# Performance work log

Measured on AMD Instinct MI355X. Metric: run time of the kernel, lower is better.

The kernel has to match this reference:

```python
import jax, jax.numpy as jnp
import numpy as np

EPS = 1e-12  # torch F.normalize eps

def _l2norm(t):
    # F.normalize(t, p=2, dim=1): divide by clamped L2 norm
    n = jnp.sqrt(jnp.sum(t * t, axis=1, keepdims=True))
    return t / jnp.maximum(n, EPS)


def setup_inputs() -> dict:
    key = jax.random.key(0)
    k1, k2, k3 = jax.random.split(key, 3)
    N, K, D = 262144, 512, 64
    inputs = jax.random.normal(k1, (N, D), dtype=jnp.float32)
    labels = jax.random.randint(k2, (N,), 0, K, dtype=jnp.int64)
    embedding = jax.random.normal(k3, (K, D), dtype=jnp.float32)
    return {"inputs": inputs, "labels": labels, "embedding": embedding}


def reference(inputs, labels, embedding):
    K, D = embedding.shape
    flat = inputs.reshape(-1, D)  # [N, D]
    # cosine similarity: [N, K]
    distances = _l2norm(flat) @ _l2norm(embedding).T
    encoding_indices = jnp.argmax(distances, axis=1)  # [N]
    encodings = jax.nn.one_hot(encoding_indices, K, dtype=flat.dtype)  # [N, K]
    # quantize lookup via one-hot matmul (as in original)
    quantized = (encodings @ embedding).reshape(inputs.shape)
    # labeled branch: closs = mean(1 - distances[i, labels[i]])
    picked = jnp.take_along_axis(distances, labels[:, None], axis=1)[:, 0]
    loss = jnp.mean(1.0 - picked)
    # straight-through estimator
    quantized = inputs + jax.lax.stop_gradient(quantized - inputs)
    perplexity = jnp.array(1, dtype=jnp.int32)
    return (loss, quantized, perplexity, encodings, encoding_indices[:, None])
```

## Files before the change

kernel.cpp:

```cpp
#include <hip/hip_runtime.h>
#include <math.h>

#define N_ROWS 262144
#define KCODES 512
#define DIM 64
#define BLOCK 256
#define ROWS_PER_BLOCK 128
#define NSUB (KCODES / 16)


typedef __attribute__((ext_vector_type(8))) short short8;
typedef __attribute__((ext_vector_type(4))) float f4;

static const size_t OFF_LOSS = 0;
static const size_t OFF_Q    = 1;
static const size_t OFF_PERP = 1 + (size_t)N_ROWS * DIM;
static const size_t OFF_ENC  = OFF_PERP + 1;
static const size_t OFF_IDX  = OFF_ENC + (size_t)N_ROWS * KCODES;

__device__ __forceinline__ unsigned short bf16rne(float f) {
    unsigned int u = __float_as_uint(f);
    u = (u + 0x7fffu + ((u >> 16) & 1u)) >> 16;
    return (unsigned short)u;
}
__device__ __forceinline__ float bf16tof(unsigned short h) {
    return __uint_as_float(((unsigned int)h) << 16);
}

__global__ __launch_bounds__(64) void vq_prep(const float* __restrict__ emb,
                                              unsigned short* __restrict__ pe,
                                              float* __restrict__ out_loss,
                                              float* __restrict__ out_perp) {
    int k = blockIdx.x;
    int d = threadIdx.x;
    float v = emb[k * DIM + d];
    float s = v * v;
    #pragma unroll
    for (int off = 32; off > 0; off >>= 1) s += __shfl_xor(s, off, 64);
    float vn = v / fmaxf(sqrtf(s), 1e-12f);
    unsigned short h = bf16rne(vn);
    float r = vn - bf16tof(h);
    unsigned short m = bf16rne(r);
    r = r - bf16tof(m);
    unsigned short l = bf16rne(r);
    int st = k >> 4, cc = k & 15;
    int ss = d >> 5, qq = (d >> 3) & 3, j = d & 7;
    int ln = qq * 16 + cc;
    pe[((size_t)(st * 6 + 0 + ss) * 64 + ln) * 8 + j] = h;
    pe[((size_t)(st * 6 + 2 + ss) * 64 + ln) * 8 + j] = m;
    pe[((size_t)(st * 6 + 4 + ss) * 64 + ln) * 8 + j] = l;
    if (k == 0 && d == 0) { *out_loss = 0.0f; *out_perp = 1.0f; }
}

#define MFMA(A, B, C) C = __builtin_amdgcn_mfma_f32_16x16x32_bf16(A, B, C, 0, 0, 0)

__global__ __launch_bounds__(BLOCK, 3) void vq_main(const float* __restrict__ x,
                                                    const int* __restrict__ labels,
                                                    const float* __restrict__ emb,
                                                    const unsigned short* __restrict__ pe,
                                                    float* __restrict__ out_loss,
                                                    float* __restrict__ out_q,
                                                    float* __restrict__ out_enc,
                                                    float* __restrict__ out_idx) {
    const int tid   = threadIdx.x;
    const int lane  = tid & 63;
    const int q     = lane >> 4;
    const int c     = lane & 15;
    const int wbase = blockIdx.x * ROWS_PER_BLOCK + (tid >> 6) * 32;

    float inv_nx[2];
    short8 Ah[2][2], Am[2][2], Al[2][2];
    #pragma unroll
    for (int t = 0; t < 2; ++t) {
        float xv[16];
        const float* xp = x + (size_t)(wbase + t * 16 + c) * DIM + q * 8;
        #pragma unroll
        for (int s = 0; s < 2; ++s) {
            float4 lo = *(const float4*)(xp + s * 32);
            float4 hi = *(const float4*)(xp + s * 32 + 4);
            xv[s * 8 + 0] = lo.x; xv[s * 8 + 1] = lo.y;
            xv[s * 8 + 2] = lo.z; xv[s * 8 + 3] = lo.w;
            xv[s * 8 + 4] = hi.x; xv[s * 8 + 5] = hi.y;
            xv[s * 8 + 6] = hi.z; xv[s * 8 + 7] = hi.w;
        }
        float s2 = 0.f;
        #pragma unroll
        for (int j = 0; j < 16; ++j) s2 = fmaf(xv[j], xv[j], s2);
        s2 += __shfl_xor(s2, 16, 64);
        s2 += __shfl_xor(s2, 32, 64);
        inv_nx[t] = 1.0f / fmaxf(sqrtf(s2), 1e-12f);
        #pragma unroll
        for (int s = 0; s < 2; ++s)
            #pragma unroll
            for (int j = 0; j < 8; ++j) {
                float v = xv[s * 8 + j];
                unsigned short h = bf16rne(v);
                float r = v - bf16tof(h);
                unsigned short m = bf16rne(r);
                r = r - bf16tof(m);
                unsigned short l = bf16rne(r);
                Ah[t][s][j] = (short)h;
                Am[t][s][j] = (short)m;
                Al[t][s][j] = (short)l;
            }
    }

    int   lbl[2][4];
    float best[2][4], pick[2][4];
    int   bidx[2][4];
    #pragma unroll
    for (int t = 0; t < 2; ++t)
        #pragma unroll
        for (int r = 0; r < 4; ++r) {
            lbl[t][r]  = labels[wbase + t * 16 + q * 4 + r];
            best[t][r] = -3.4e38f;
            bidx[t][r] = 0;
            pick[t][r] = 0.f;
        }

    #pragma unroll 2
    for (int st = 0; st < NSUB; ++st) {
        const unsigned short* bp = pe + ((size_t)st * 6 * 64 + lane) * 8;
        short8 Bh0 = *(const short8*)(bp);
        short8 Bh1 = *(const short8*)(bp + 512);
        short8 Bm0 = *(const short8*)(bp + 1024);
        short8 Bm1 = *(const short8*)(bp + 1536);
        short8 Bl0 = *(const short8*)(bp + 2048);
        short8 Bl1 = *(const short8*)(bp + 2560);

        {
            float* zb = out_enc + (size_t)(wbase + st) * KCODES;
            f4 z = {0.f, 0.f, 0.f, 0.f};
            __builtin_nontemporal_store(z, (f4*)(zb + lane * 4));
            __builtin_nontemporal_store(z, (f4*)(zb + 256 + lane * 4));
        }

        f4 acc0 = {0.f, 0.f, 0.f, 0.f};
        f4 acc1 = {0.f, 0.f, 0.f, 0.f};
        MFMA(Ah[0][0], Bh0, acc0);  MFMA(Ah[1][0], Bh0, acc1);
        MFMA(Ah[0][1], Bh1, acc0);  MFMA(Ah[1][1], Bh1, acc1);
        MFMA(Ah[0][0], Bm0, acc0);  MFMA(Ah[1][0], Bm0, acc1);
        MFMA(Ah[0][1], Bm1, acc0);  MFMA(Ah[1][1], Bm1, acc1);
        MFMA(Am[0][0], Bh0, acc0);  MFMA(Am[1][0], Bh0, acc1);
        MFMA(Am[0][1], Bh1, acc0);  MFMA(Am[1][1], Bh1, acc1);
        MFMA(Ah[0][0], Bl0, acc0);  MFMA(Ah[1][0], Bl0, acc1);
        MFMA(Ah[0][1], Bl1, acc0);  MFMA(Ah[1][1], Bl1, acc1);
        MFMA(Al[0][0], Bh0, acc0);  MFMA(Al[1][0], Bh0, acc1);
        MFMA(Al[0][1], Bh1, acc0);  MFMA(Al[1][1], Bh1, acc1);
        MFMA(Am[0][0], Bm0, acc0);  MFMA(Am[1][0], Bm0, acc1);
        MFMA(Am[0][1], Bm1, acc0);  MFMA(Am[1][1], Bm1, acc1);

        const int code = st * 16 + c;
        #pragma unroll
        for (int r = 0; r < 4; ++r) {
            float d0 = acc0[r];
            if (d0 > best[0][r]) { best[0][r] = d0; bidx[0][r] = code; }
            if (code == lbl[0][r]) pick[0][r] = d0;
            float d1 = acc1[r];
            if (d1 > best[1][r]) { best[1][r] = d1; bidx[1][r] = code; }
            if (code == lbl[1][r]) pick[1][r] = d1;
        }
    }

    asm volatile("s_waitcnt vmcnt(0)" ::: "memory");

    #pragma unroll
    for (int t = 0; t < 2; ++t)
        #pragma unroll
        for (int r = 0; r < 4; ++r) {
            float b = best[t][r]; int i = bidx[t][r]; float p = pick[t][r];
            #pragma unroll
            for (int m = 1; m < 16; m <<= 1) {
                float ob = __shfl_xor(b, m, 64);
                int   oi = __shfl_xor(i, m, 64);
                p += __shfl_xor(p, m, 64);
                if (ob > b || (ob == b && oi < i)) { b = ob; i = oi; }
            }
            bidx[t][r] = i; pick[t][r] = p;
        }

    if (c == 0) {
        #pragma unroll
        for (int t = 0; t < 2; ++t)
            #pragma unroll
            for (int r = 0; r < 4; ++r) {
                int row = wbase + t * 16 + q * 4 + r;
                out_enc[(size_t)row * KCODES + bidx[t][r]] = 1.0f;
                out_idx[row] = (float)bidx[t][r];
            }
    }

    #pragma unroll
    for (int t = 0; t < 2; ++t)
        #pragma unroll
        for (int r = 0; r < 4; ++r) {
            int row = wbase + t * 16 + q * 4 + r;
            f4 v = ((const f4*)(emb + (size_t)bidx[t][r] * DIM))[c];
            __builtin_nontemporal_store(v, ((f4*)(out_q + (size_t)row * DIM)) + c);
        }

    float lv = 0.f;
    #pragma unroll
    for (int t = 0; t < 2; ++t)
        #pragma unroll
        for (int r = 0; r < 4; ++r) {
            float invv = __shfl(inv_nx[t], q * 4 + r, 64);
            lv += (1.0f - pick[t][r] * invv);
        }
    lv *= 1.0f / ((float)N_ROWS * 16.0f);
    #pragma unroll
    for (int m = 1; m < 64; m <<= 1) lv += __shfl_xor(lv, m, 64);
    if (lane == 0) atomicAdd(out_loss, lv);
}

extern "C" void kernel_launch(void* const* d_in, const int* in_sizes, int n_in,
                              void* d_out, int out_size, void* d_ws, size_t ws_size,
                              hipStream_t stream) {
    const float* x      = (const float*)d_in[0];
    const int*   labels = (const int*)d_in[1];
    const float* emb    = (const float*)d_in[2];
    float* out = (float*)d_out;
    unsigned short* pe = (unsigned short*)d_ws;

    hipLaunchKernelGGL(vq_prep, dim3(KCODES), dim3(64), 0, stream,
                       emb, pe, out + OFF_LOSS, out + OFF_PERP);
    hipLaunchKernelGGL(vq_main, dim3(N_ROWS / ROWS_PER_BLOCK), dim3(BLOCK), 0, stream,
                       x, labels, emb, pe,
                       out + OFF_LOSS, out + OFF_Q, out + OFF_ENC, out + OFF_IDX);
}
```

Baseline: 718.2 us.

## Stage codebook tiles in LDS and write one-hot rows after argmax

Codebook fragments are now loaded cooperatively into shared memory in stages of four 16-code subtiles, with block barriers, instead of each wave reading them from global memory. The separate zero-fill stores plus scattered 1.0 store for the encodings matrix become one pass that writes each one-hot row directly once the argmax is known. Occupancy hint raised from 3 to 6 blocks per SM. The aim is to cut redundant global/L2 traffic and remove the overlapping zero-then-set writes, at the cost of synchronization stalls, and it no longer overlaps the large encoding writes with the MFMA loop.

```diff
diff --git a/kernel.cpp b/kernel.cpp
--- a/kernel.cpp
+++ b/kernel.cpp
@@ -6,7 +6,10 @@
 #define DIM 64
 #define BLOCK 256
 #define ROWS_PER_BLOCK 128
-#define NSUB (KCODES / 16)
+#define NSUB 32
+#define SUBS_PER_STAGE 4
+#define NSTAGES (NSUB / SUBS_PER_STAGE)
+#define STAGE_USHORTS (SUBS_PER_STAGE * 6 * 64 * 8)
 
 
 typedef __attribute__((ext_vector_type(8))) short short8;
@@ -54,7 +57,7 @@
 
 #define MFMA(A, B, C) C = __builtin_amdgcn_mfma_f32_16x16x32_bf16(A, B, C, 0, 0, 0)
 
-__global__ __launch_bounds__(BLOCK, 3) void vq_main(const float* __restrict__ x,
+__global__ __launch_bounds__(BLOCK, 6) void vq_main(const float* __restrict__ x,
                                                     const int* __restrict__ labels,
                                                     const float* __restrict__ emb,
                                                     const unsigned short* __restrict__ pe,
@@ -68,6 +71,8 @@
     const int c     = lane & 15;
     const int wbase = blockIdx.x * ROWS_PER_BLOCK + (tid >> 6) * 32;
 
+    __shared__ __align__(16) unsigned short sE[STAGE_USHORTS];
+
     float inv_nx[2];
     short8 Ah[2][2], Am[2][2], Al[2][2];
     #pragma unroll
@@ -118,51 +123,55 @@
             pick[t][r] = 0.f;
         }
 
-    #pragma unroll 2
-    for (int st = 0; st < NSUB; ++st) {
-        const unsigned short* bp = pe + ((size_t)st * 6 * 64 + lane) * 8;
-        short8 Bh0 = *(const short8*)(bp);
-        short8 Bh1 = *(const short8*)(bp + 512);
-        short8 Bm0 = *(const short8*)(bp + 1024);
-        short8 Bm1 = *(const short8*)(bp + 1536);
-        short8 Bl0 = *(const short8*)(bp + 2048);
-        short8 Bl1 = *(const short8*)(bp + 2560);
-
+    for (int stg = 0; stg < NSTAGES; ++stg) {
+        __syncthreads();
         {
-            float* zb = out_enc + (size_t)(wbase + st) * KCODES;
-            f4 z = {0.f, 0.f, 0.f, 0.f};
-            __builtin_nontemporal_store(z, (f4*)(zb + lane * 4));
-            __builtin_nontemporal_store(z, (f4*)(zb + 256 + lane * 4));
-        }
-
-        f4 acc0 = {0.f, 0.f, 0.f, 0.f};
-        f4 acc1 = {0.f, 0.f, 0.f, 0.f};
-        MFMA(Ah[0][0], Bh0, acc0);  MFMA(Ah[1][0], Bh0, acc1);
-        MFMA(Ah[0][1], Bh1, acc0);  MFMA(Ah[1][1], Bh1, acc1);
-        MFMA(Ah[0][0], Bm0, acc0);  MFMA(Ah[1][0], Bm0, acc1);
-        MFMA(Ah[0][1], Bm1, acc0);  MFMA(Ah[1][1], Bm1, acc1);
-        MFMA(Am[0][0], Bh0, acc0);  MFMA(Am[1][0], Bh0, acc1);
-        MFMA(Am[0][1], Bh1, acc0);  MFMA(Am[1][1], Bh1, acc1);
-        MFMA(Ah[0][0], Bl0, acc0);  MFMA(Ah[1][0], Bl0, acc1);
-        MFMA(Ah[0][1], Bl1, acc0);  MFMA(Ah[1][1], Bl1, acc1);
-        MFMA(Al[0][0], Bh0, acc0);  MFMA(Al[1][0], Bh0, acc1);
-        MFMA(Al[0][1], Bh1, acc0);  MFMA(Al[1][1], Bh1, acc1);
-        MFMA(Am[0][0], Bm0, acc0);  MFMA(Am[1][0], Bm0, acc1);
-        MFMA(Am[0][1], Bm1, acc0);  MFMA(Am[1][1], Bm1, acc1);
-
-        const int code = st * 16 + c;
-        #pragma unroll
-        for (int r = 0; r < 4; ++r) {
-            float d0 = acc0[r];
-            if (d0 > best[0][r]) { best[0][r] = d0; bidx[0][r] = code; }
-            if (code == lbl[0][r]) pick[0][r] = d0;
-            float d1 = acc1[r];
-            if (d1 > best[1][r]) { best[1][r] = d1; bidx[1][r] = code; }
-            if (code == lbl[1][r]) pick[1][r] = d1;
-        }
-    }
-
-    asm volatile("s_waitcnt vmcnt(0)" ::: "memory");
+            const unsigned short* src = pe + (size_t)stg * STAGE_USHORTS;
+            #pragma unroll
+            for (int i = 0; i < 6; ++i) {
+                int ch = tid + i * BLOCK;
+                *(f4*)&sE[ch * 8] = *(const f4*)(src + ch * 8);
+            }
+        }
+        __syncthreads();
+
+        #pragma unroll
+        for (int sub = 0; sub < SUBS_PER_STAGE; ++sub) {
+            const unsigned short* bp = &sE[((sub * 6) * 64 + lane) * 8];
+            short8 Bh0 = *(const short8*)(bp);
+            short8 Bh1 = *(const short8*)(bp + 512);
+            short8 Bm0 = *(const short8*)(bp + 1024);
+            short8 Bm1 = *(const short8*)(bp + 1536);
+            short8 Bl0 = *(const short8*)(bp + 2048);
+            short8 Bl1 = *(const short8*)(bp + 2560);
+
+            f4 acc0 = {0.f, 0.f, 0.f, 0.f};
+            f4 acc1 = {0.f, 0.f, 0.f, 0.f};
+            MFMA(Ah[0][0], Bh0, acc0);  MFMA(Ah[1][0], Bh0, acc1);
+            MFMA(Ah[0][1], Bh1, acc0);  MFMA(Ah[1][1], Bh1, acc1);
+            MFMA(Ah[0][0], Bm0, acc0);  MFMA(Ah[1][0], Bm0, acc1);
+            MFMA(Ah[0][1], Bm1, acc0);  MFMA(Ah[1][1], Bm1, acc1);
+            MFMA(Am[0][0], Bh0, acc0);  MFMA(Am[1][0], Bh0, acc1);
+            MFMA(Am[0][1], Bh1, acc0);  MFMA(Am[1][1], Bh1, acc1);
+            MFMA(Ah[0][0], Bl0, acc0);  MFMA(Ah[1][0], Bl0, acc1);
+            MFMA(Ah[0][1], Bl1, acc0);  MFMA(Ah[1][1], Bl1, acc1);
+            MFMA(Al[0][0], Bh0, acc0);  MFMA(Al[1][0], Bh0, acc1);
+            MFMA(Al[0][1], Bh1, acc0);  MFMA(Al[1][1], Bh1, acc1);
+            MFMA(Am[0][0], Bm0, acc0);  MFMA(Am[1][0], Bm0, acc1);
+            MFMA(Am[0][1], Bm1, acc0);  MFMA(Am[1][1], Bm1, acc1);
+
+            const int code = (stg * SUBS_PER_STAGE + sub) * 16 + c;
+            #pragma unroll
+            for (int r = 0; r < 4; ++r) {
+                float d0 = acc0[r];
+                if (d0 > best[0][r]) { best[0][r] = d0; bidx[0][r] = code; }
+                if (code == lbl[0][r]) pick[0][r] = d0;
+                float d1 = acc1[r];
+                if (d1 > best[1][r]) { best[1][r] = d1; bidx[1][r] = code; }
+                if (code == lbl[1][r]) pick[1][r] = d1;
+            }
+        }
+    }
 
     #pragma unroll
     for (int t = 0; t < 2; ++t)
@@ -179,13 +188,31 @@
             bidx[t][r] = i; pick[t][r] = p;
         }
 
+    {
+        const int col0 = lane * 4, col1 = 256 + lane * 4;
+        #pragma unroll
+        for (int r32 = 0; r32 < 32; ++r32) {
+            int bi = __shfl(bidx[r32 >> 4][r32 & 3], ((r32 >> 2) & 3) * 16, 64);
+            float* base = out_enc + (size_t)(wbase + r32) * KCODES;
+            f4 v0 = { bi == col0     ? 1.f : 0.f,
+                      bi == col0 + 1 ? 1.f : 0.f,
+                      bi == col0 + 2 ? 1.f : 0.f,
+                      bi == col0 + 3 ? 1.f : 0.f };
+            __builtin_nontemporal_store(v0, (f4*)(base + col0));
+            f4 v1 = { bi == col1     ? 1.f : 0.f,
+                      bi == col1 + 1 ? 1.f : 0.f,
+                      bi == col1 + 2 ? 1.f : 0.f,
+                      bi == col1 + 3 ? 1.f : 0.f };
+            __builtin_nontemporal_store(v1, (f4*)(base + col1));
+        }
+    }
+
     if (c == 0) {
         #pragma unroll
         for (int t = 0; t < 2; ++t)
             #pragma unroll
             for (int r = 0; r < 4; ++r) {
                 int row = wbase + t * 16 + q * 4 + r;
-                out_enc[(size_t)row * KCODES + bidx[t][r]] = 1.0f;
                 out_idx[row] = (float)bidx[t][r];
             }
     }
```

Result: slower. 1.251 ms (+74.1%).
